# Optimization experiments

Hardware: AMD Instinct MI355X
Metric: run time of the kernel (lower is better)

## Reference

```python
import jax, jax.numpy as jnp
import numpy as np
import math

B, T, C = 8, 2048, 512
N_HEAD, N_ATTN, MAXLEN, N_LAYER, LAYER_ID = 8, 512, 2048, 12, 6
HEAD_SIZE = N_ATTN // N_HEAD


def setup_inputs() -> dict:
    key = jax.random.key(0)
    ks = jax.random.split(key, 12)
    # ---- time_w per __init__ formula ----
    curve = -(MAXLEN - 1 - np.arange(MAXLEN)).astype(np.float32)
    ww = np.ones((N_HEAD, MAXLEN), dtype=np.float32)
    for h in range(N_HEAD):
        if h < N_HEAD - 1:
            decay_speed = math.pow(MAXLEN, -(h + 1) / (N_HEAD - 1))
        else:
            decay_speed = 0.0
        ww[h] = np.exp(curve * decay_speed)
    time_w = jnp.asarray(ww)
    # ---- time_mix per __init__ formula ----
    ratio_0_to_1 = LAYER_ID / (N_LAYER - 1)
    ratio_1_to_almost0 = 1.0 - LAYER_ID / N_LAYER
    base = (np.arange(C, dtype=np.float32) / C).reshape(1, 1, C)
    time_mix_k = jnp.asarray(np.power(base, ratio_1_to_almost0))
    time_mix_v = jnp.asarray(np.power(base, ratio_1_to_almost0) + 0.3 * ratio_0_to_1)
    time_mix_r = jnp.asarray(np.power(base, 0.5 * ratio_1_to_almost0))
    # ---- alpha/beta/gamma (init at ones, small perturbation for nontrivial grads) ----
    time_alpha = 1.0 + 0.05 * jax.random.normal(ks[0], (N_HEAD, 1, MAXLEN), jnp.float32)
    time_beta = 1.0 + 0.05 * jax.random.normal(ks[1], (N_HEAD, MAXLEN, 1), jnp.float32)
    time_gamma = 1.0 + 0.05 * jax.random.normal(ks[2], (MAXLEN, 1), jnp.float32)
    s = 0.02
    return {
        "x": jax.random.normal(ks[3], (B, T, C), jnp.float32),
        "time_w": time_w,
        "time_alpha": time_alpha,
        "time_beta": time_beta,
        "time_gamma": time_gamma,
        "time_mix_k": time_mix_k,
        "time_mix_v": time_mix_v,
        "time_mix_r": time_mix_r,
        "Wk": s * jax.random.normal(ks[4], (N_ATTN, C), jnp.float32),
        "bk": jnp.zeros((N_ATTN,), jnp.float32),
        "Wv": s * jax.random.normal(ks[5], (N_ATTN, C), jnp.float32),
        "bv": jnp.zeros((N_ATTN,), jnp.float32),
        "Wr": s * jax.random.normal(ks[6], (N_ATTN, C), jnp.float32),
        "br": jnp.zeros((N_ATTN,), jnp.float32),
        "Wo": s * jax.random.normal(ks[7], (C, N_ATTN), jnp.float32),
        "bo": jnp.zeros((C,), jnp.float32),
    }


def reference(x, time_w, time_alpha, time_beta, time_gamma,
              time_mix_k, time_mix_v, time_mix_r,
              Wk, bk, Wv, bv, Wr, br, Wo, bo):
    Bc, Tc, Cc = x.shape
    H, TT = time_w.shape
    hs = Wk.shape[0] // H
    # Toeplitz causal decay matrix: w[h,t,u] = time_w[h, TT-1-(t-u)] for u<=t else 0
    t = jnp.arange(Tc)
    diff = t[:, None] - t[None, :]                      # [T,T]
    idx = jnp.clip(TT - 1 - diff, 0, TT - 1)
    w = jnp.where(diff >= 0, time_w[:, idx], 0.0)       # [H,T,T]
    w = w * time_alpha[:, :, :Tc] * time_beta[:, :Tc, :]
    # time shift: xx[:,t] = x[:,t-1], xx[:,0] = 0
    xx = jnp.pad(x, ((0, 0), (1, 0), (0, 0)))[:, :Tc]
    xk = x * time_mix_k + xx * (1.0 - time_mix_k)
    xv = x * time_mix_v + xx * (1.0 - time_mix_v)
    xr = x * time_mix_r + xx * (1.0 - time_mix_r)
    k = xk @ Wk.T + bk
    v = xv @ Wv.T + bv
    r = xr @ Wr.T + br
    k = jnp.exp(jnp.clip(k, -60.0, 30.0))
    sum_k = jnp.cumsum(k, axis=1)                        # [B,T,A]
    kv = (k * v).reshape(Bc, Tc, H, hs)                  # [B,T,H,hs]
    wkv = jnp.einsum('htu,buhc->bthc', w, kv).reshape(Bc, Tc, -1)
    rwkv = jax.nn.sigmoid(r) * wkv / sum_k
    out = rwkv @ Wo.T + bo
    return out * time_gamma[:Tc, :]
```

## Files before the change

### kernel.cpp

```cpp
#include <hip/hip_runtime.h>
#include <hip/hip_bf16.h>

#define TTLEN 2048
#define NCH   64
#define CLEN  32

typedef unsigned short ushort_t;
typedef __attribute__((ext_vector_type(8))) short short8;
typedef __attribute__((ext_vector_type(4))) float f32x4;

__device__ __forceinline__ unsigned short f2bf(float f) {
    __hip_bfloat16 h = __float2bfloat16(f);
    return *reinterpret_cast<unsigned short*>(&h);
}
__device__ __forceinline__ float bf2f(unsigned int u16) {
    union { unsigned int i; float f; } v; v.i = u16 << 16; return v.f;
}

#define GLD_LDS16(gp, lp) __builtin_amdgcn_global_load_lds( \
    (const __attribute__((address_space(1))) void*)(gp),    \
    (__attribute__((address_space(3))) void*)(lp), 16, 0, 0)

__global__ void convert4(const float* __restrict__ Wk, const float* __restrict__ Wv,
                         const float* __restrict__ Wr, const float* __restrict__ Wo,
                         ushort_t* __restrict__ Wall, ushort_t* __restrict__ Wob) {
    int m = blockIdx.x >> 8;
    const float* src = (m == 0) ? Wk : (m == 1) ? Wv : (m == 2) ? Wr : Wo;
    ushort_t* dst = (m == 3) ? Wob : Wall + (size_t)m * 262144;
    int i = (blockIdx.x & 255) * 256 + threadIdx.x;
    float4 v = *(const float4*)(src + (size_t)i * 4);
    union { unsigned short u[4]; uint2 p; } pk;
    pk.u[0] = f2bf(v.x); pk.u[1] = f2bf(v.y); pk.u[2] = f2bf(v.z); pk.u[3] = f2bf(v.w);
    *(uint2*)(dst + (size_t)i * 4) = pk.p;
}

__global__ void mix3(const float* __restrict__ x,
                     const float* __restrict__ tmk, const float* __restrict__ tmv,
                     const float* __restrict__ tmr,
                     ushort_t* __restrict__ xk, ushort_t* __restrict__ xv,
                     ushort_t* __restrict__ xr) {
    int i   = blockIdx.x * 256 + threadIdx.x;
    int c4  = (i & 127) << 2;
    int row = i >> 7;
    int t   = row & (TTLEN - 1);
    float4 xc = *(const float4*)(x + (size_t)row * 512 + c4);
    float4 xp = make_float4(0.f, 0.f, 0.f, 0.f);
    if (t != 0) xp = *(const float4*)(x + (size_t)(row - 1) * 512 + c4);
    size_t o = (size_t)row * 512 + c4;
    union { unsigned short u[4]; uint2 p; } pk;
    {
        float4 tv = *(const float4*)(tmk + c4);
        pk.u[0] = f2bf(xc.x * tv.x + xp.x * (1.f - tv.x));
        pk.u[1] = f2bf(xc.y * tv.y + xp.y * (1.f - tv.y));
        pk.u[2] = f2bf(xc.z * tv.z + xp.z * (1.f - tv.z));
        pk.u[3] = f2bf(xc.w * tv.w + xp.w * (1.f - tv.w));
        *(uint2*)(xk + o) = pk.p;
    }
    {
        float4 tv = *(const float4*)(tmv + c4);
        pk.u[0] = f2bf(xc.x * tv.x + xp.x * (1.f - tv.x));
        pk.u[1] = f2bf(xc.y * tv.y + xp.y * (1.f - tv.y));
        pk.u[2] = f2bf(xc.z * tv.z + xp.z * (1.f - tv.z));
        pk.u[3] = f2bf(xc.w * tv.w + xp.w * (1.f - tv.w));
        *(uint2*)(xv + o) = pk.p;
    }
    {
        float4 tv = *(const float4*)(tmr + c4);
        pk.u[0] = f2bf(xc.x * tv.x + xp.x * (1.f - tv.x));
        pk.u[1] = f2bf(xc.y * tv.y + xp.y * (1.f - tv.y));
        pk.u[2] = f2bf(xc.z * tv.z + xp.z * (1.f - tv.z));
        pk.u[3] = f2bf(xc.w * tv.w + xp.w * (1.f - tv.w));
        *(uint2*)(xr + o) = pk.p;
    }
}

template <int MODE>
__launch_bounds__(512, 4)
__global__ void gemm_big(const ushort_t* __restrict__ Axk, const ushort_t* __restrict__ Axv,
                         const ushort_t* __restrict__ Axr, const ushort_t* __restrict__ W,
                         const float* __restrict__ b0, const float* __restrict__ b1,
                         const float* __restrict__ b2,
                         ushort_t* __restrict__ o0, ushort_t* __restrict__ o1,
                         ushort_t* __restrict__ o2,
                         float* __restrict__ fout, const float* __restrict__ gamma) {
    __shared__ alignas(16) ushort_t As[128 * 64];
    __shared__ alignas(16) ushort_t Bs[256 * 64];
    const int tid  = threadIdx.x;
    const int lane = tid & 63;
    const int w    = tid >> 6;
    const int wm   = (w >> 2) << 6;
    const int wn   = (w & 3) << 6;
    const int mBlk = blockIdx.y << 7;
    const int nBlk = blockIdx.x << 8;
    const int r16  = lane & 15, q = lane >> 4;
    const int rowInW = lane >> 3, ch = lane & 7;

    const int p = (MODE == 0) ? (blockIdx.x >> 1) : 0;
    const ushort_t* A = (MODE == 1) ? Axk : (p == 0 ? Axk : (p == 1 ? Axv : Axr));

    f32x4 acc[4][4];
#pragma unroll
    for (int a = 0; a < 4; ++a)
#pragma unroll
        for (int b = 0; b < 4; ++b) acc[a][b] = (f32x4){0.f, 0.f, 0.f, 0.f};

    for (int k0 = 0; k0 < 512; k0 += 64) {
        const ushort_t* Ag = A + (size_t)mBlk * 512 + k0;
        const ushort_t* Bg = W + (size_t)nBlk * 512 + k0;
#pragma unroll
        for (int i = 0; i < 2; ++i) {
            int baseRow = w * 16 + i * 8;
            int row = baseRow + rowInW;
            int gch = ch ^ (row & 7);
            GLD_LDS16(Ag + (size_t)row * 512 + gch * 8, &As[baseRow * 64]);
        }
#pragma unroll
        for (int i = 0; i < 4; ++i) {
            int baseRow = w * 32 + i * 8;
            int row = baseRow + rowInW;
            int gch = ch ^ (row & 7);
            GLD_LDS16(Bg + (size_t)row * 512 + gch * 8, &Bs[baseRow * 64]);
        }
        asm volatile("s_waitcnt vmcnt(0)" ::: "memory");
        __syncthreads();
#pragma unroll
        for (int s = 0; s < 2; ++s) {
            short8 af[4], bfr[4];
#pragma unroll
            for (int mt = 0; mt < 4; ++mt) {
                int row = wm + mt * 16 + r16;
                af[mt] = *(const short8*)(&As[row * 64 + (((s * 4 + q) ^ (r16 & 7)) << 3)]);
            }
#pragma unroll
            for (int nt = 0; nt < 4; ++nt) {
                int row = wn + nt * 16 + r16;
                bfr[nt] = *(const short8*)(&Bs[row * 64 + (((s * 4 + q) ^ (r16 & 7)) << 3)]);
            }
#pragma unroll
            for (int mt = 0; mt < 4; ++mt)
#pragma unroll
                for (int nt = 0; nt < 4; ++nt)
                    acc[mt][nt] = __builtin_amdgcn_mfma_f32_16x16x32_bf16(
                        af[mt], bfr[nt], acc[mt][nt], 0, 0, 0);
        }
        __syncthreads();
    }

    if (MODE == 0) {
        const float* bias = (p == 0) ? b0 : (p == 1) ? b1 : b2;
        ushort_t* outp = (p == 0) ? o0 : (p == 1) ? o1 : o2;
#pragma unroll
        for (int mt = 0; mt < 4; ++mt) {
#pragma unroll
            for (int nt = 0; nt < 4; ++nt) {
                int nLocal = (nBlk & 511) + wn + nt * 16 + r16;
                float bv = bias[nLocal];
#pragma unroll
                for (int i = 0; i < 4; ++i) {
                    int row = mBlk + wm + mt * 16 + (q << 2) + i;
                    float v = acc[mt][nt][i] + bv;
                    if (p == 0) v = __expf(fminf(fmaxf(v, -60.f), 30.f));
                    else if (p == 2) v = 1.f / (1.f + __expf(-v));
                    outp[(size_t)row * 512 + nLocal] = f2bf(v);
                }
            }
        }
    } else {
#pragma unroll
        for (int mt = 0; mt < 4; ++mt) {
#pragma unroll
            for (int nt = 0; nt < 4; ++nt) {
                int col = nBlk + wn + nt * 16 + r16;
                float bv = b0[col];
#pragma unroll
                for (int i = 0; i < 4; ++i) {
                    int row = mBlk + wm + mt * 16 + (q << 2) + i;
                    float v = (acc[mt][nt][i] + bv) * gamma[row & (TTLEN - 1)];
                    fout[(size_t)row * 512 + col] = v;
                }
            }
        }
    }
}

__global__ void scanA(const ushort_t* __restrict__ kb, const ushort_t* __restrict__ vb,
                      const float* __restrict__ tw, const float* __restrict__ alpha,
                      float* __restrict__ Sloc, float* __restrict__ Kloc) {
    int b = blockIdx.x >> 6, j = blockIdx.x & 63;
    int a0 = threadIdx.x * 4;
    int h = a0 >> 6;
    float r = tw[h * TTLEN + TTLEN - 2];
    int t0 = j * CLEN;
    size_t base = ((size_t)(b * TTLEN + t0)) * 512 + a0;
    const float* al = alpha + h * TTLEN + t0;
    float s[4] = {0.f, 0.f, 0.f, 0.f}, sk[4] = {0.f, 0.f, 0.f, 0.f};
#pragma unroll 8
    for (int it = 0; it < CLEN; ++it) {
        uint2 kk = *(const uint2*)(kb + base + (size_t)it * 512);
        uint2 vv = *(const uint2*)(vb + base + (size_t)it * 512);
        float kf[4] = {bf2f(kk.x & 0xffff), bf2f(kk.x >> 16),
                       bf2f(kk.y & 0xffff), bf2f(kk.y >> 16)};
        float vf[4] = {bf2f(vv.x & 0xffff), bf2f(vv.x >> 16),
                       bf2f(vv.y & 0xffff), bf2f(vv.y >> 16)};
        float av = al[it];
#pragma unroll
        for (int c = 0; c < 4; ++c) {
            sk[c] += kf[c];
            s[c] = fmaf(r, s[c], av * kf[c] * vf[c]);
        }
    }
    int o = (b * NCH + j) * 512 + a0;
    *(float4*)(Sloc + o) = make_float4(s[0], s[1], s[2], s[3]);
    *(float4*)(Kloc + o) = make_float4(sk[0], sk[1], sk[2], sk[3]);
}

__global__ void scanMid(const float* __restrict__ tw,
                        const float* __restrict__ Sloc, const float* __restrict__ Kloc,
                        float* __restrict__ Sin, float* __restrict__ Kin) {
    int idx = blockIdx.x * 256 + threadIdx.x;
    int a = idx & 511, b = idx >> 9;
    int h = a >> 6;
    float r = tw[h * TTLEN + TTLEN - 2];
    float rL = r;
#pragma unroll
    for (int i = 0; i < 5; ++i) rL *= rL;
    float cs = 0.f, ck = 0.f;
#pragma unroll
    for (int j = 0; j < NCH; ++j) {
        int o = (b * NCH + j) * 512 + a;
        Sin[o] = cs; Kin[o] = ck;
        cs = fmaf(rL, cs, Sloc[o]);
        ck += Kloc[o];
    }
}

__global__ void scanB(const ushort_t* __restrict__ kb, const ushort_t* __restrict__ vb,
                      const ushort_t* __restrict__ rb,
                      const float* __restrict__ tw, const float* __restrict__ alpha,
                      const float* __restrict__ beta,
                      const float* __restrict__ Sin, const float* __restrict__ Kin,
                      ushort_t* __restrict__ rwkv) {
    int b = blockIdx.x >> 6, j = blockIdx.x & 63;
    int a0 = threadIdx.x * 4;
    int h = a0 >> 6;
    float r = tw[h * TTLEN + TTLEN - 2];
    int t0 = j * CLEN;
    size_t base = ((size_t)(b * TTLEN + t0)) * 512 + a0;
    const float* al = alpha + h * TTLEN + t0;
    const float* bt = beta + h * TTLEN + t0;
    int o = (b * NCH + j) * 512 + a0;
    float4 sv = *(const float4*)(Sin + o);
    float4 kv = *(const float4*)(Kin + o);
    float s[4] = {sv.x, sv.y, sv.z, sv.w};
    float sk[4] = {kv.x, kv.y, kv.z, kv.w};
#pragma unroll 4
    for (int it = 0; it < CLEN; ++it) {
        uint2 kk = *(const uint2*)(kb + base + (size_t)it * 512);
        uint2 vv = *(const uint2*)(vb + base + (size_t)it * 512);
        uint2 rr = *(const uint2*)(rb + base + (size_t)it * 512);
        float kf[4] = {bf2f(kk.x & 0xffff), bf2f(kk.x >> 16),
                       bf2f(kk.y & 0xffff), bf2f(kk.y >> 16)};
        float vf[4] = {bf2f(vv.x & 0xffff), bf2f(vv.x >> 16),
                       bf2f(vv.y & 0xffff), bf2f(vv.y >> 16)};
        float rf[4] = {bf2f(rr.x & 0xffff), bf2f(rr.x >> 16),
                       bf2f(rr.y & 0xffff), bf2f(rr.y >> 16)};
        float av = al[it], btv = bt[it];
        unsigned short u[4];
#pragma unroll
        for (int c = 0; c < 4; ++c) {
            sk[c] += kf[c];
            s[c] = fmaf(r, s[c], av * kf[c] * vf[c]);
            u[c] = f2bf(rf[c] * btv * s[c] / sk[c]);
        }
        uint2 outw;
        outw.x = ((unsigned int)u[1] << 16) | u[0];
        outw.y = ((unsigned int)u[3] << 16) | u[2];
        *(uint2*)(rwkv + base + (size_t)it * 512) = outw;
    }
}

extern "C" void kernel_launch(void* const* d_in, const int* in_sizes, int n_in,
                              void* d_out, int out_size, void* d_ws, size_t ws_size,
                              hipStream_t stream) {
    const float* x   = (const float*)d_in[0];
    const float* tw  = (const float*)d_in[1];
    const float* ta  = (const float*)d_in[2];
    const float* tb  = (const float*)d_in[3];
    const float* tg  = (const float*)d_in[4];
    const float* tmk = (const float*)d_in[5];
    const float* tmv = (const float*)d_in[6];
    const float* tmr = (const float*)d_in[7];
    const float* Wk  = (const float*)d_in[8];
    const float* bk  = (const float*)d_in[9];
    const float* Wv  = (const float*)d_in[10];
    const float* bv  = (const float*)d_in[11];
    const float* Wr  = (const float*)d_in[12];
    const float* br  = (const float*)d_in[13];
    const float* Wo  = (const float*)d_in[14];
    const float* bo  = (const float*)d_in[15];

    char* ws = (char*)d_ws;
    ushort_t* Wall = (ushort_t*)(ws + 0);
    ushort_t* Wob  = (ushort_t*)(ws + 1572864);
    ushort_t* xk   = (ushort_t*)(ws + 2097152);
    ushort_t* xv   = (ushort_t*)(ws + 18874368);
    ushort_t* xr   = (ushort_t*)(ws + 35651584);
    ushort_t* kb   = (ushort_t*)(ws + 52428800);
    ushort_t* vb   = (ushort_t*)(ws + 69206016);
    ushort_t* rb   = (ushort_t*)(ws + 85983232);
    ushort_t* rwkv = xk;
    float* Sloc = (float*)(ws + 102760448);
    float* Kloc = (float*)(ws + 103809024);
    float* Sin  = (float*)(ws + 104857600);
    float* Kin  = (float*)(ws + 105906176);

    convert4<<<1024, 256, 0, stream>>>(Wk, Wv, Wr, Wo, Wall, Wob);
    mix3<<<8192, 256, 0, stream>>>(x, tmk, tmv, tmr, xk, xv, xr);

    gemm_big<0><<<dim3(6, 128), 512, 0, stream>>>(xk, xv, xr, Wall, bk, bv, br,
                                                  kb, vb, rb, nullptr, nullptr);

    scanA<<<512, 128, 0, stream>>>(kb, vb, tw, ta, Sloc, Kloc);
    scanMid<<<16, 256, 0, stream>>>(tw, Sloc, Kloc, Sin, Kin);
    scanB<<<512, 128, 0, stream>>>(kb, vb, rb, tw, ta, tb, Sin, Kin, rwkv);

    gemm_big<1><<<dim3(2, 128), 512, 0, stream>>>(rwkv, nullptr, nullptr, Wob, bo, nullptr,
                                                  nullptr, nullptr, nullptr, nullptr,
                                                  (float*)d_out, tg);
}
```

Before: 214.4 us.

## Fuse prep kernels, enlarge QKV GEMM tile, fuse scan via decoupled lookback

Merges the weight conversion, token-mix and flag-reset kernels into one prep launch. Widens the K/V/R projection GEMM to 256x256 tiles and halves its occupancy hint. Replaces the three-pass chunked scan (local, mid, apply) with one kernel in which each chunk publishes its local state and flag, then walks back over earlier chunks' published states before applying its own. The aim is fewer launches and less intermediate traffic, at the cost of spin-waiting, which assumes earlier blocks are scheduled first, and more register pressure in the GEMM.

```diff
diff --git a/kernel.cpp b/kernel.cpp
--- a/kernel.cpp
+++ b/kernel.cpp
@@ -21,25 +21,31 @@
     (const __attribute__((address_space(1))) void*)(gp),    \
     (__attribute__((address_space(3))) void*)(lp), 16, 0, 0)
 
-__global__ void convert4(const float* __restrict__ Wk, const float* __restrict__ Wv,
-                         const float* __restrict__ Wr, const float* __restrict__ Wo,
-                         ushort_t* __restrict__ Wall, ushort_t* __restrict__ Wob) {
-    int m = blockIdx.x >> 8;
-    const float* src = (m == 0) ? Wk : (m == 1) ? Wv : (m == 2) ? Wr : Wo;
-    ushort_t* dst = (m == 3) ? Wob : Wall + (size_t)m * 262144;
-    int i = (blockIdx.x & 255) * 256 + threadIdx.x;
-    float4 v = *(const float4*)(src + (size_t)i * 4);
-    union { unsigned short u[4]; uint2 p; } pk;
-    pk.u[0] = f2bf(v.x); pk.u[1] = f2bf(v.y); pk.u[2] = f2bf(v.z); pk.u[3] = f2bf(v.w);
-    *(uint2*)(dst + (size_t)i * 4) = pk.p;
-}
-
-__global__ void mix3(const float* __restrict__ x,
+__global__ void prep(const float* __restrict__ Wk, const float* __restrict__ Wv,
+                     const float* __restrict__ Wr, const float* __restrict__ Wo,
+                     ushort_t* __restrict__ Wall, ushort_t* __restrict__ Wob,
+                     const float* __restrict__ x,
                      const float* __restrict__ tmk, const float* __restrict__ tmv,
                      const float* __restrict__ tmr,
                      ushort_t* __restrict__ xk, ushort_t* __restrict__ xv,
-                     ushort_t* __restrict__ xr) {
-    int i   = blockIdx.x * 256 + threadIdx.x;
+                     ushort_t* __restrict__ xr, int* __restrict__ flags) {
+    if (blockIdx.x == 9216) {
+        flags[threadIdx.x] = 0;
+        flags[threadIdx.x + 256] = 0;
+        return;
+    }
+    if (blockIdx.x < 1024) {
+        int m = blockIdx.x >> 8;
+        const float* src = (m == 0) ? Wk : (m == 1) ? Wv : (m == 2) ? Wr : Wo;
+        ushort_t* dst = (m == 3) ? Wob : Wall + (size_t)m * 262144;
+        int i = (blockIdx.x & 255) * 256 + threadIdx.x;
+        float4 v = *(const float4*)(src + (size_t)i * 4);
+        union { unsigned short u[4]; uint2 p; } pk;
+        pk.u[0] = f2bf(v.x); pk.u[1] = f2bf(v.y); pk.u[2] = f2bf(v.z); pk.u[3] = f2bf(v.w);
+        *(uint2*)(dst + (size_t)i * 4) = pk.p;
+        return;
+    }
+    int i   = (blockIdx.x - 1024) * 256 + threadIdx.x;
     int c4  = (i & 127) << 2;
     int row = i >> 7;
     int t   = row & (TTLEN - 1);
@@ -74,15 +80,95 @@
     }
 }
 
-template <int MODE>
-__launch_bounds__(512, 4)
-__global__ void gemm_big(const ushort_t* __restrict__ Axk, const ushort_t* __restrict__ Axv,
-                         const ushort_t* __restrict__ Axr, const ushort_t* __restrict__ W,
-                         const float* __restrict__ b0, const float* __restrict__ b1,
-                         const float* __restrict__ b2,
-                         ushort_t* __restrict__ o0, ushort_t* __restrict__ o1,
-                         ushort_t* __restrict__ o2,
-                         float* __restrict__ fout, const float* __restrict__ gamma) {
+__launch_bounds__(512, 2)
+__global__ void gemm256(const ushort_t* __restrict__ Axk, const ushort_t* __restrict__ Axv,
+                        const ushort_t* __restrict__ Axr, const ushort_t* __restrict__ W,
+                        const float* __restrict__ b0, const float* __restrict__ b1,
+                        const float* __restrict__ b2,
+                        ushort_t* __restrict__ o0, ushort_t* __restrict__ o1,
+                        ushort_t* __restrict__ o2) {
+    __shared__ alignas(16) ushort_t As[256 * 64];
+    __shared__ alignas(16) ushort_t Bs[256 * 64];
+    const int tid  = threadIdx.x;
+    const int lane = tid & 63;
+    const int w    = tid >> 6;
+    const int wm   = (w >> 1) << 6;
+    const int wn   = (w & 1) << 7;
+    const int mBlk = blockIdx.y << 8;
+    const int nBlk = blockIdx.x << 8;
+    const int r16  = lane & 15, q = lane >> 4;
+    const int rowInW = lane >> 3, ch = lane & 7;
+
+    const int p = blockIdx.x >> 1;
+    const ushort_t* A = (p == 0) ? Axk : (p == 1) ? Axv : Axr;
+
+    f32x4 acc[4][8];
+#pragma unroll
+    for (int a = 0; a < 4; ++a)
+#pragma unroll
+        for (int b = 0; b < 8; ++b) acc[a][b] = (f32x4){0.f, 0.f, 0.f, 0.f};
+
+    for (int k0 = 0; k0 < 512; k0 += 64) {
+        const ushort_t* Ag = A + (size_t)mBlk * 512 + k0;
+        const ushort_t* Bg = W + (size_t)nBlk * 512 + k0;
+#pragma unroll
+        for (int i = 0; i < 4; ++i) {
+            int baseRow = w * 32 + i * 8;
+            int row = baseRow + rowInW;
+            int gch = ch ^ (row & 7);
+            GLD_LDS16(Ag + (size_t)row * 512 + gch * 8, &As[baseRow * 64]);
+            GLD_LDS16(Bg + (size_t)row * 512 + gch * 8, &Bs[baseRow * 64]);
+        }
+        asm volatile("s_waitcnt vmcnt(0)" ::: "memory");
+        __syncthreads();
+#pragma unroll
+        for (int s = 0; s < 2; ++s) {
+            short8 af[4], bfr[8];
+#pragma unroll
+            for (int mt = 0; mt < 4; ++mt) {
+                int row = wm + mt * 16 + r16;
+                af[mt] = *(const short8*)(&As[row * 64 + (((s * 4 + q) ^ (r16 & 7)) << 3)]);
+            }
+#pragma unroll
+            for (int nt = 0; nt < 8; ++nt) {
+                int row = wn + nt * 16 + r16;
+                bfr[nt] = *(const short8*)(&Bs[row * 64 + (((s * 4 + q) ^ (r16 & 7)) << 3)]);
+            }
+#pragma unroll
+            for (int mt = 0; mt < 4; ++mt)
+#pragma unroll
+                for (int nt = 0; nt < 8; ++nt)
+                    acc[mt][nt] = __builtin_amdgcn_mfma_f32_16x16x32_bf16(
+                        af[mt], bfr[nt], acc[mt][nt], 0, 0, 0);
+        }
+        __syncthreads();
+    }
+
+    const float* bias = (p == 0) ? b0 : (p == 1) ? b1 : b2;
+    ushort_t* outp = (p == 0) ? o0 : (p == 1) ? o1 : o2;
+    const int nBase = (blockIdx.x & 1) << 8;
+#pragma unroll
+    for (int mt = 0; mt < 4; ++mt) {
+#pragma unroll
+        for (int nt = 0; nt < 8; ++nt) {
+            int nLocal = nBase + wn + nt * 16 + r16;
+            float bv = bias[nLocal];
+#pragma unroll
+            for (int i = 0; i < 4; ++i) {
+                int row = mBlk + wm + mt * 16 + (q << 2) + i;
+                float v = acc[mt][nt][i] + bv;
+                if (p == 0) v = __expf(fminf(fmaxf(v, -60.f), 30.f));
+                else if (p == 2) v = 1.f / (1.f + __expf(-v));
+                outp[(size_t)row * 512 + nLocal] = f2bf(v);
+            }
+        }
+    }
+}
+
+__launch_bounds__(512, 2)
+__global__ void gemm_out(const ushort_t* __restrict__ Arw, const ushort_t* __restrict__ W,
+                         const float* __restrict__ bo, float* __restrict__ fout,
+                         const float* __restrict__ gamma) {
     __shared__ alignas(16) ushort_t As[128 * 64];
     __shared__ alignas(16) ushort_t Bs[256 * 64];
     const int tid  = threadIdx.x;
@@ -95,9 +181,6 @@
     const int r16  = lane & 15, q = lane >> 4;
     const int rowInW = lane >> 3, ch = lane & 7;
 
-    const int p = (MODE == 0) ? (blockIdx.x >> 1) : 0;
-    const ushort_t* A = (MODE == 1) ? Axk : (p == 0 ? Axk : (p == 1 ? Axv : Axr));
-
     f32x4 acc[4][4];
 #pragma unroll
     for (int a = 0; a < 4; ++a)
@@ -105,7 +188,7 @@
         for (int b = 0; b < 4; ++b) acc[a][b] = (f32x4){0.f, 0.f, 0.f, 0.f};
 
     for (int k0 = 0; k0 < 512; k0 += 64) {
-        const ushort_t* Ag = A + (size_t)mBlk * 512 + k0;
+        const ushort_t* Ag = Arw + (size_t)mBlk * 512 + k0;
         const ushort_t* Bg = W + (size_t)nBlk * 512 + k0;
 #pragma unroll
         for (int i = 0; i < 2; ++i) {
@@ -146,53 +229,40 @@
         __syncthreads();
     }
 
-    if (MODE == 0) {
-        const float* bias = (p == 0) ? b0 : (p == 1) ? b1 : b2;
-        ushort_t* outp = (p == 0) ? o0 : (p == 1) ? o1 : o2;
-#pragma unroll
-        for (int mt = 0; mt < 4; ++mt) {
-#pragma unroll
-            for (int nt = 0; nt < 4; ++nt) {
-                int nLocal = (nBlk & 511) + wn + nt * 16 + r16;
-                float bv = bias[nLocal];
-#pragma unroll
-                for (int i = 0; i < 4; ++i) {
-                    int row = mBlk + wm + mt * 16 + (q << 2) + i;
-                    float v = acc[mt][nt][i] + bv;
-                    if (p == 0) v = __expf(fminf(fmaxf(v, -60.f), 30.f));
-                    else if (p == 2) v = 1.f / (1.f + __expf(-v));
-                    outp[(size_t)row * 512 + nLocal] = f2bf(v);
-                }
-            }
-        }
-    } else {
-#pragma unroll
-        for (int mt = 0; mt < 4; ++mt) {
-#pragma unroll
-            for (int nt = 0; nt < 4; ++nt) {
-                int col = nBlk + wn + nt * 16 + r16;
-                float bv = b0[col];
-#pragma unroll
-                for (int i = 0; i < 4; ++i) {
-                    int row = mBlk + wm + mt * 16 + (q << 2) + i;
-                    float v = (acc[mt][nt][i] + bv) * gamma[row & (TTLEN - 1)];
-                    fout[(size_t)row * 512 + col] = v;
-                }
-            }
-        }
-    }
-}
-
-__global__ void scanA(const ushort_t* __restrict__ kb, const ushort_t* __restrict__ vb,
-                      const float* __restrict__ tw, const float* __restrict__ alpha,
-                      float* __restrict__ Sloc, float* __restrict__ Kloc) {
-    int b = blockIdx.x >> 6, j = blockIdx.x & 63;
-    int a0 = threadIdx.x * 4;
-    int h = a0 >> 6;
-    float r = tw[h * TTLEN + TTLEN - 2];
-    int t0 = j * CLEN;
-    size_t base = ((size_t)(b * TTLEN + t0)) * 512 + a0;
+#pragma unroll
+    for (int mt = 0; mt < 4; ++mt) {
+#pragma unroll
+        for (int nt = 0; nt < 4; ++nt) {
+            int col = nBlk + wn + nt * 16 + r16;
+            float bv = bo[col];
+#pragma unroll
+            for (int i = 0; i < 4; ++i) {
+                int row = mBlk + wm + mt * 16 + (q << 2) + i;
+                float v = (acc[mt][nt][i] + bv) * gamma[row & (TTLEN - 1)];
+                fout[(size_t)row * 512 + col] = v;
+            }
+        }
+    }
+}
+
+__global__ void scan_fused(const ushort_t* __restrict__ kb, const ushort_t* __restrict__ vb,
+                           const ushort_t* __restrict__ rb,
+                           const float* __restrict__ tw, const float* __restrict__ alpha,
+                           const float* __restrict__ beta,
+                           float* __restrict__ Sloc, float* __restrict__ Kloc,
+                           int* __restrict__ flags, ushort_t* __restrict__ rwkv) {
+    const int b = blockIdx.x >> 6, j = blockIdx.x & 63;
+    const int a0 = threadIdx.x * 4;
+    const int h = a0 >> 6;
+    const float r = tw[h * TTLEN + TTLEN - 2];
+    float rL = r;
+#pragma unroll
+    for (int i = 0; i < 5; ++i) rL *= rL;
+    const int t0 = j * CLEN;
+    const size_t base = ((size_t)(b * TTLEN + t0)) * 512 + a0;
     const float* al = alpha + h * TTLEN + t0;
+    const float* bt = beta + h * TTLEN + t0;
+
     float s[4] = {0.f, 0.f, 0.f, 0.f}, sk[4] = {0.f, 0.f, 0.f, 0.f};
 #pragma unroll 8
     for (int it = 0; it < CLEN; ++it) {
@@ -209,50 +279,35 @@
             s[c] = fmaf(r, s[c], av * kf[c] * vf[c]);
         }
     }
-    int o = (b * NCH + j) * 512 + a0;
-    *(float4*)(Sloc + o) = make_float4(s[0], s[1], s[2], s[3]);
-    *(float4*)(Kloc + o) = make_float4(sk[0], sk[1], sk[2], sk[3]);
-}
-
-__global__ void scanMid(const float* __restrict__ tw,
-                        const float* __restrict__ Sloc, const float* __restrict__ Kloc,
-                        float* __restrict__ Sin, float* __restrict__ Kin) {
-    int idx = blockIdx.x * 256 + threadIdx.x;
-    int a = idx & 511, b = idx >> 9;
-    int h = a >> 6;
-    float r = tw[h * TTLEN + TTLEN - 2];
-    float rL = r;
-#pragma unroll
-    for (int i = 0; i < 5; ++i) rL *= rL;
-    float cs = 0.f, ck = 0.f;
-#pragma unroll
-    for (int j = 0; j < NCH; ++j) {
-        int o = (b * NCH + j) * 512 + a;
-        Sin[o] = cs; Kin[o] = ck;
-        cs = fmaf(rL, cs, Sloc[o]);
-        ck += Kloc[o];
-    }
-}
-
-__global__ void scanB(const ushort_t* __restrict__ kb, const ushort_t* __restrict__ vb,
-                      const ushort_t* __restrict__ rb,
-                      const float* __restrict__ tw, const float* __restrict__ alpha,
-                      const float* __restrict__ beta,
-                      const float* __restrict__ Sin, const float* __restrict__ Kin,
-                      ushort_t* __restrict__ rwkv) {
-    int b = blockIdx.x >> 6, j = blockIdx.x & 63;
-    int a0 = threadIdx.x * 4;
-    int h = a0 >> 6;
-    float r = tw[h * TTLEN + TTLEN - 2];
-    int t0 = j * CLEN;
-    size_t base = ((size_t)(b * TTLEN + t0)) * 512 + a0;
-    const float* al = alpha + h * TTLEN + t0;
-    const float* bt = beta + h * TTLEN + t0;
-    int o = (b * NCH + j) * 512 + a0;
-    float4 sv = *(const float4*)(Sin + o);
-    float4 kv = *(const float4*)(Kin + o);
-    float s[4] = {sv.x, sv.y, sv.z, sv.w};
-    float sk[4] = {kv.x, kv.y, kv.z, kv.w};
+    {
+        int o = blockIdx.x * 512 + a0;
+        *(float4*)(Sloc + o) = make_float4(s[0], s[1], s[2], s[3]);
+        *(float4*)(Kloc + o) = make_float4(sk[0], sk[1], sk[2], sk[3]);
+    }
+    __syncthreads();
+    if (threadIdx.x == 0) {
+        __threadfence();
+        __hip_atomic_store(&flags[blockIdx.x], 1, __ATOMIC_RELEASE, __HIP_MEMORY_SCOPE_AGENT);
+    }
+
+    float cs[4] = {0.f, 0.f, 0.f, 0.f}, ck[4] = {0.f, 0.f, 0.f, 0.f};
+    float f = 1.f;
+    for (int p = j - 1; p >= 0; --p) {
+        int pc = (b << 6) + p;
+        while (__hip_atomic_load(&flags[pc], __ATOMIC_ACQUIRE, __HIP_MEMORY_SCOPE_AGENT) == 0) {
+            __builtin_amdgcn_s_sleep(1);
+        }
+        int o = pc * 512 + a0;
+        float4 S = *(const float4*)(Sloc + o);
+        float4 K = *(const float4*)(Kloc + o);
+        cs[0] = fmaf(f, S.x, cs[0]); cs[1] = fmaf(f, S.y, cs[1]);
+        cs[2] = fmaf(f, S.z, cs[2]); cs[3] = fmaf(f, S.w, cs[3]);
+        ck[0] += K.x; ck[1] += K.y; ck[2] += K.z; ck[3] += K.w;
+        f *= rL;
+    }
+
+    float ss[4] = {cs[0], cs[1], cs[2], cs[3]};
+    float kk2[4] = {ck[0], ck[1], ck[2], ck[3]};
 #pragma unroll 4
     for (int it = 0; it < CLEN; ++it) {
         uint2 kk = *(const uint2*)(kb + base + (size_t)it * 512);
@@ -268,9 +323,9 @@
         unsigned short u[4];
 #pragma unroll
         for (int c = 0; c < 4; ++c) {
-            sk[c] += kf[c];
-            s[c] = fmaf(r, s[c], av * kf[c] * vf[c]);
-            u[c] = f2bf(rf[c] * btv * s[c] / sk[c]);
+            kk2[c] += kf[c];
+            ss[c] = fmaf(r, ss[c], av * kf[c] * vf[c]);
+            u[c] = f2bf(rf[c] * btv * ss[c] / kk2[c]);
         }
         uint2 outw;
         outw.x = ((unsigned int)u[1] << 16) | u[0];
@@ -311,20 +366,16 @@
     ushort_t* rwkv = xk;
     float* Sloc = (float*)(ws + 102760448);
     float* Kloc = (float*)(ws + 103809024);
-    float* Sin  = (float*)(ws + 104857600);
-    float* Kin  = (float*)(ws + 105906176);
-
-    convert4<<<1024, 256, 0, stream>>>(Wk, Wv, Wr, Wo, Wall, Wob);
-    mix3<<<8192, 256, 0, stream>>>(x, tmk, tmv, tmr, xk, xv, xr);
-
-    gemm_big<0><<<dim3(6, 128), 512, 0, stream>>>(xk, xv, xr, Wall, bk, bv, br,
-                                                  kb, vb, rb, nullptr, nullptr);
-
-    scanA<<<512, 128, 0, stream>>>(kb, vb, tw, ta, Sloc, Kloc);
-    scanMid<<<16, 256, 0, stream>>>(tw, Sloc, Kloc, Sin, Kin);
-    scanB<<<512, 128, 0, stream>>>(kb, vb, rb, tw, ta, tb, Sin, Kin, rwkv);
-
-    gemm_big<1><<<dim3(2, 128), 512, 0, stream>>>(rwkv, nullptr, nullptr, Wob, bo, nullptr,
-                                                  nullptr, nullptr, nullptr, nullptr,
-                                                  (float*)d_out, tg);
-}
+    int*   flags = (int*)(ws + 104857600);
+
+    prep<<<9217, 256, 0, stream>>>(Wk, Wv, Wr, Wo, Wall, Wob,
+                                   x, tmk, tmv, tmr, xk, xv, xr, flags);
+
+    gemm256<<<dim3(6, 64), 512, 0, stream>>>(xk, xv, xr, Wall, bk, bv, br,
+                                             kb, vb, rb);
+
+    scan_fused<<<512, 128, 0, stream>>>(kb, vb, rb, tw, ta, tb,
+                                        Sloc, Kloc, flags, rwkv);
+
+    gemm_out<<<dim3(2, 128), 512, 0, stream>>>(rwkv, Wob, bo, (float*)d_out, tg);
+}
```

After: 496.9 us. 2.32x slower.
